# Kernel tuning notes

Measured on AMD Instinct MI355X. Metric: run time of the kernel, lower is better.

Reference implementation:

```python
import jax, jax.numpy as jnp
import numpy as np

N, E, IN, HID, H = 20000, 320000, 256, 128, 4
NEG_SLOPE = 0.2
BN_EPS = 1e-5


def _glorot(k, shape):
    lim = float(np.sqrt(6.0 / (shape[0] + shape[-1])))
    return jax.random.uniform(k, shape, jnp.float32, -lim, lim)


def setup_inputs() -> dict:
    key = jax.random.key(0)
    ks = jax.random.split(key, 16)
    x = jax.random.normal(ks[0], (N, IN), jnp.float32)
    src = jax.random.randint(ks[1], (E,), 0, N, jnp.int32)
    dst = jax.random.randint(ks[2], (E,), 0, N, jnp.int32)
    dst = jnp.where(dst == src, (dst + 1) % N, dst)  # no pre-existing self-loops
    edge_index = jnp.stack([src, dst])
    p = {}
    i = 3
    for l, fin in [(0, IN), (1, HID)]:
        p[f"Wl{l}"] = _glorot(ks[i], (fin, H * HID)); i += 1
        p[f"Wr{l}"] = _glorot(ks[i], (fin, H * HID)); i += 1
        p[f"bl{l}"] = jnp.zeros((H * HID,), jnp.float32)
        p[f"br{l}"] = jnp.zeros((H * HID,), jnp.float32)
        p[f"att{l}"] = _glorot(ks[i], (H, HID)); i += 1
        p[f"b{l}"] = jnp.zeros((HID,), jnp.float32)
        p[f"g{l}"] = jnp.ones((HID,), jnp.float32)
        p[f"be{l}"] = jnp.zeros((HID,), jnp.float32)
    p["skip_W"] = _glorot(ks[i], (IN, HID))
    p["skip_b"] = jnp.zeros((HID,), jnp.float32)
    return {"x": x, "edge_index": edge_index, **p}


def _gatv2(x, src, dst, Wl, bl, Wr, br, att, b, n):
    # PyG GATv2Conv, heads=H, concat=False (mean over heads), eval mode (no dropout)
    xl = (x @ Wl + bl).reshape(n, H, HID)   # lin_l (source)
    xr = (x @ Wr + br).reshape(n, H, HID)   # lin_r (target)
    m = xl[src] + xr[dst]                   # [Etot,H,C]
    e = jnp.einsum('ehc,hc->eh', jax.nn.leaky_relu(m, NEG_SLOPE), att)
    emax = jax.ops.segment_max(e, dst, num_segments=n)
    a = jnp.exp(e - emax[dst])
    denom = jax.ops.segment_sum(a, dst, num_segments=n)
    alpha = a / denom[dst]                  # per-target softmax over incoming edges
    out = jax.ops.segment_sum(alpha[:, :, None] * xl[src], dst, num_segments=n)
    return out.mean(axis=1) + b


def _bn(x, g, be):
    # BatchNorm1d, training-mode batch statistics (biased variance)
    mu = x.mean(0)
    var = x.var(0)
    return (x - mu) * jax.lax.rsqrt(var + BN_EPS) * g + be


def reference(x, edge_index, Wl0, Wr0, bl0, br0, att0, b0, g0, be0,
              Wl1, Wr1, bl1, br1, att1, b1, g1, be1, skip_W, skip_b):
    n = x.shape[0]
    loop = jnp.arange(n, dtype=edge_index.dtype)  # add_self_loops (GATv2 default)
    src = jnp.concatenate([edge_index[0], loop])
    dst = jnp.concatenate([edge_index[1], loop])
    h = x @ skip_W + skip_b
    out = _gatv2(x, src, dst, Wl0, bl0, Wr0, br0, att0, b0, n)
    out = _bn(jax.nn.leaky_relu(out, NEG_SLOPE), g0, be0) + h
    out = _gatv2(out, src, dst, Wl1, bl1, Wr1, br1, att1, b1, n)
    out = _bn(jax.nn.leaky_relu(out, NEG_SLOPE), g1, be1)
    return out
```

## Files before the change

kernel.cpp:

```cpp
#include <hip/hip_runtime.h>
#include <math.h>

#define NEG 0.2f
#define BN_EPS 1e-5f
#define LOG2E 1.44269504088896340736f

typedef __attribute__((ext_vector_type(8))) short  bf16x8;
typedef __attribute__((ext_vector_type(4))) float  f32x4;

__device__ inline unsigned short f2b(float f) {
    unsigned int u = __float_as_uint(f);
    unsigned int r = (u + 0x7fffu + ((u >> 16) & 1u)) >> 16;
    return (unsigned short)r;
}
__device__ inline float b2f_lo(unsigned int u) { return __uint_as_float(u << 16); }
__device__ inline float b2f_hi(unsigned int u) { return __uint_as_float(u & 0xffff0000u); }

__device__ inline unsigned int cvt_pk_bf16(float lo, float hi) {
    unsigned int r;
    asm("v_cvt_pk_bf16_f32 %0, %1, %2" : "=v"(r) : "v"(lo), "v"(hi));
    return r;
}

template<int CTRL>
__device__ inline float dpp_add(float x) {
    int y = __builtin_amdgcn_update_dpp(0, __float_as_int(x), CTRL, 0xF, 0xF, true);
    return x + __int_as_float(y);
}

__global__ void hist_kernel(const int* __restrict__ dst, int* __restrict__ counts, int E4) {
    int i = blockIdx.x * 256 + threadIdx.x;
    if (i >= E4) return;
    int4 d = ((const int4*)dst)[i];
    atomicAdd(&counts[d.x], 1);
    atomicAdd(&counts[d.y], 1);
    atomicAdd(&counts[d.z], 1);
    atomicAdd(&counts[d.w], 1);
}

__global__ void pscan_kernel(const int* __restrict__ counts, int* __restrict__ offsets,
                             int* __restrict__ btot, int n) {
    __shared__ int wsums[16];
    int tid = threadIdx.x, wid = tid >> 6, lane = tid & 63;
    int i = blockIdx.x * 1024 + tid;
    int v = (i < n) ? counts[i] + 1 : 0;
    int incl = v;
#pragma unroll
    for (int off = 1; off < 64; off <<= 1) {
        int t = __shfl_up(incl, off);
        if (lane >= off) incl += t;
    }
    if (lane == 63) wsums[wid] = incl;
    __syncthreads();
    if (tid < 16) {
        int wv = wsums[tid];
        int winc = wv;
#pragma unroll
        for (int off = 1; off < 16; off <<= 1) {
            int t = __shfl_up(winc, off);
            if (tid >= off) winc += t;
        }
        wsums[tid] = winc - wv;
        if (tid == 15) btot[blockIdx.x] = winc;
    }
    __syncthreads();
    if (i < n) offsets[i] = wsums[wid] + incl - v;
}

__global__ void addb_kernel(int* __restrict__ offsets, const int* __restrict__ btot,
                            int n, int nb) {
    __shared__ int sbase;
    if (threadIdx.x == 0) {
        int b = 0, t = 0;
        for (int j = 0; j < nb; ++j) {
            int v = btot[j];
            if (j < (int)blockIdx.x) b += v;
            t += v;
        }
        sbase = b;
        if (blockIdx.x == (unsigned)(nb - 1)) offsets[n] = t;
    }
    __syncthreads();
    int i = blockIdx.x * 1024 + threadIdx.x;
    if (i < n) offsets[i] += sbase;
}

__global__ void scatter_kernel(const int* __restrict__ src, const int* __restrict__ dst,
                               const int* __restrict__ offsets, int* __restrict__ cursor,
                               int* __restrict__ csr_src, int E, int N) {
    int i = blockIdx.x * 256 + threadIdx.x;
    if (i < E) {
        int d = dst[i];
        int pos = offsets[d] + 1 + atomicAdd(&cursor[d], 1);
        csr_src[pos] = src[i];
    } else if (i < E + N) {
        int n = i - E;
        csr_src[offsets[n]] = n;
    }
}

__device__ inline void pack_body(const float* __restrict__ W, unsigned short* __restrict__ Ap,
                                 int K, int Nsrc, int fn_off, int t) {
    int KS = K >> 5;
    int lane = t & 63;
    int frag = t >> 6;
    int ks = frag % KS;
    int nb = frag / KS;
    int fn = fn_off + nb;
    int k0 = ks * 32 + (lane >> 4) * 8;
    int col = nb * 16 + (lane & 15);
    unsigned short o[8];
#pragma unroll
    for (int j = 0; j < 8; ++j) o[j] = f2b(W[(size_t)(k0 + j) * Nsrc + col]);
    *(uint4*)&Ap[(((size_t)fn * KS + ks) * 64 + lane) * 8] = *(uint4*)o;
}

__global__ void prep_kernel(const float* __restrict__ x, unsigned short* __restrict__ xb,
                            const float* __restrict__ Wl0, const float* __restrict__ Wr0,
                            const float* __restrict__ skW, const float* __restrict__ Wl1,
                            const float* __restrict__ Wr1,
                            unsigned short* __restrict__ Ap0, unsigned short* __restrict__ Ap1,
                            const float* __restrict__ bl0, const float* __restrict__ br0,
                            const float* __restrict__ skb, const float* __restrict__ bl1,
                            const float* __restrict__ br1,
                            float* __restrict__ bias0f, float* __restrict__ bias1f, int N) {
    const int CONV = (N * 256 / 8) / 256;
    int b = blockIdx.x, tid = threadIdx.x;
    if (b < CONV) {
        int i = b * 256 + tid;
        const float4* p = (const float4*)&x[(size_t)i * 8];
        float4 a = p[0], c = p[1];
        unsigned short o[8];
        o[0] = f2b(a.x); o[1] = f2b(a.y); o[2] = f2b(a.z); o[3] = f2b(a.w);
        o[4] = f2b(c.x); o[5] = f2b(c.y); o[6] = f2b(c.z); o[7] = f2b(c.w);
        *(uint4*)&xb[(size_t)i * 8] = *(uint4*)o;
        return;
    }
    b -= CONV;
    if (b < 64)  { pack_body(Wl0, Ap0, 256, 512, 0,  b * 256 + tid); return; }
    b -= 64;
    if (b < 64)  { pack_body(Wr0, Ap0, 256, 512, 32, b * 256 + tid); return; }
    b -= 64;
    if (b < 16)  { pack_body(skW, Ap0, 256, 128, 64, b * 256 + tid); return; }
    b -= 16;
    if (b < 32)  { pack_body(Wl1, Ap1, 128, 512, 0,  b * 256 + tid); return; }
    b -= 32;
    if (b < 32)  { pack_body(Wr1, Ap1, 128, 512, 32, b * 256 + tid); return; }
    b -= 32;
    {
        int i = b * 256 + tid;
        if (i < 1152) {
            float v = (i < 512) ? bl0[i] : (i < 1024 ? br0[i - 512] : skb[i - 1024]);
            bias0f[i] = v;
        } else if (i < 1152 + 1024) {
            int j = i - 1152;
            bias1f[j] = (j < 512) ? bl1[j] : br1[j - 512];
        }
    }
}

__global__ __launch_bounds__(256) void gemm_nt(
    const unsigned short* __restrict__ Bx, const unsigned short* __restrict__ Ap,
    const float* __restrict__ bias, unsigned short* __restrict__ out,
    int Mnodes, int Ncols, int K) {
    int wid = threadIdx.x >> 6, lane = threadIdx.x & 63;
    int g = lane >> 4, c15 = lane & 15;
    int cfbase = blockIdx.y * 8 + (wid & 1) * 4;
    int ch0 = cfbase * 16;
    int nodeBase = blockIdx.x * 256 + (wid >> 1) * 128;
    const int KS = K >> 5;

    f32x4 acc[4][8];
#pragma unroll
    for (int i = 0; i < 4; ++i)
#pragma unroll
        for (int j = 0; j < 8; ++j) acc[i][j] = (f32x4){0.f, 0.f, 0.f, 0.f};

    int nd[8];
    const unsigned short* brow[8];
#pragma unroll
    for (int nf = 0; nf < 8; ++nf) {
        int n = nodeBase + nf * 16 + c15;
        nd[nf] = n;
        int nc = n < Mnodes ? n : Mnodes - 1;
        brow[nf] = Bx + (size_t)nc * K + g * 8;
    }

    for (int ks = 0; ks < KS; ++ks) {
        int koff = ks * 32;
        bf16x8 a[4];
#pragma unroll
        for (int mf = 0; mf < 4; ++mf)
            a[mf] = *(const bf16x8*)&Ap[(((size_t)(cfbase + mf) * KS + ks) * 64 + lane) * 8];
        bf16x8 b[8];
#pragma unroll
        for (int nf = 0; nf < 8; ++nf)
            b[nf] = *(const bf16x8*)(brow[nf] + koff);
#pragma unroll
        for (int nf = 0; nf < 8; ++nf)
#pragma unroll
            for (int mf = 0; mf < 4; ++mf)
                acc[mf][nf] = __builtin_amdgcn_mfma_f32_16x16x32_bf16(a[mf], b[nf], acc[mf][nf], 0, 0, 0);
    }
#pragma unroll
    for (int mf = 0; mf < 4; ++mf) {
        int ch = ch0 + mf * 16 + g * 4;
        float4 bs = *(const float4*)&bias[ch];
#pragma unroll
        for (int nf = 0; nf < 8; ++nf) {
            f32x4 v = acc[mf][nf];
            unsigned int p0 = cvt_pk_bf16(v[0] + bs.x, v[1] + bs.y);
            unsigned int p1 = cvt_pk_bf16(v[2] + bs.z, v[3] + bs.w);
            if (nd[nf] < Mnodes)
                *(uint2*)&out[(size_t)nd[nf] * Ncols + ch] = make_uint2(p0, p1);
        }
    }
}

__global__ __launch_bounds__(128) void gat_edge_kernel(
    const int* __restrict__ offsets, const int* __restrict__ csr_src,
    const unsigned short* __restrict__ base, int stride,
    const float* __restrict__ att, const float* __restrict__ bvec,
    float* __restrict__ prebn, int N) {
    int lane = threadIdx.x & 63;
    int n = blockIdx.x * 2 + (threadIdx.x >> 6);
    if (n >= N) return;
    int start = offsets[n], e1 = offsets[n + 1] - 1;
    float xrv[8], ca[8], cb[8], bv[8];
    {
        uint4 u = *(const uint4*)&base[(size_t)n * stride + 512 + lane * 8];
        xrv[0] = b2f_lo(u.x); xrv[1] = b2f_hi(u.x);
        xrv[2] = b2f_lo(u.y); xrv[3] = b2f_hi(u.y);
        xrv[4] = b2f_lo(u.z); xrv[5] = b2f_hi(u.z);
        xrv[6] = b2f_lo(u.w); xrv[7] = b2f_hi(u.w);
        const float4* q = (const float4*)&att[lane * 8];
        float4 u0 = q[0], u1 = q[1];
        const float sA = 0.6f * LOG2E, sB = 0.4f * LOG2E;
        ca[0] = u0.x * sA; ca[1] = u0.y * sA; ca[2] = u0.z * sA; ca[3] = u0.w * sA;
        ca[4] = u1.x * sA; ca[5] = u1.y * sA; ca[6] = u1.z * sA; ca[7] = u1.w * sA;
        cb[0] = u0.x * sB; cb[1] = u0.y * sB; cb[2] = u0.z * sB; cb[3] = u0.w * sB;
        cb[4] = u1.x * sB; cb[5] = u1.y * sB; cb[6] = u1.z * sB; cb[7] = u1.w * sB;
        if (lane < 16) {
            const float4* bp = (const float4*)&bvec[lane * 8];
            float4 b0 = bp[0], b1 = bp[1];
            bv[0] = b0.x; bv[1] = b0.y; bv[2] = b0.z; bv[3] = b0.w;
            bv[4] = b1.x; bv[5] = b1.y; bv[6] = b1.z; bv[7] = b1.w;
        }
    }
    float m = -INFINITY, d = 0.f;
    float acc[8] = {0, 0, 0, 0, 0, 0, 0, 0};

    const int lofs = lane * 8;
    auto LD = [&](int j) -> uint4 {
        int jj = j < e1 ? j : e1;
        int s = csr_src[jj];
        return *(const uint4*)&base[(size_t)s * stride + lofs];
    };
    auto PROC = [&](const uint4& Q) {
        float v[8];
        v[0] = b2f_lo(Q.x); v[1] = b2f_hi(Q.x);
        v[2] = b2f_lo(Q.y); v[3] = b2f_hi(Q.y);
        v[4] = b2f_lo(Q.z); v[5] = b2f_hi(Q.z);
        v[6] = b2f_lo(Q.w); v[7] = b2f_hi(Q.w);
        float p = 0.f;
#pragma unroll
        for (int j = 0; j < 8; ++j) {
            float t = v[j] + xrv[j];
            p = fmaf(ca[j], t, fmaf(cb[j], fabsf(t), p));
        }
        p = dpp_add<0xB1>(p);
        p = dpp_add<0x4E>(p);
        p = dpp_add<0x141>(p);
        p = dpp_add<0x140>(p);
        if (__any(p > m)) {
            float mn = fmaxf(m, p);
            float scale = exp2f(m - mn);
            float w = exp2f(p - mn);
            d = fmaf(d, scale, w);
#pragma unroll
            for (int j = 0; j < 8; ++j) acc[j] = fmaf(w, v[j], acc[j] * scale);
            m = mn;
        } else {
            float w = exp2f(p - m);
            d += w;
#pragma unroll
            for (int j = 0; j < 8; ++j) acc[j] = fmaf(w, v[j], acc[j]);
        }
    };

    uint4 q0 = LD(start), q1 = LD(start + 1), q2 = LD(start + 2), q3 = LD(start + 3);
    int i = start;
    for (;;) {
        PROC(q0); if (++i > e1) break; q0 = LD(i + 3);
        PROC(q1); if (++i > e1) break; q1 = LD(i + 3);
        PROC(q2); if (++i > e1) break; q2 = LD(i + 3);
        PROC(q3); if (++i > e1) break; q3 = LD(i + 3);
    }

    float inv = 1.f / d;
    float t[8];
#pragma unroll
    for (int j = 0; j < 8; ++j) {
        float u = acc[j] * inv;
        u += __shfl_xor(u, 16);
        u += __shfl_xor(u, 32);
        t[j] = u;
    }
    if (lane < 16) {
        float o[8];
#pragma unroll
        for (int j = 0; j < 8; ++j) {
            float v2 = 0.25f * t[j] + bv[j];
            o[j] = v2 > 0.f ? v2 : NEG * v2;
        }
        float* dstp = &prebn[(size_t)n * 128 + lane * 8];
        *(float4*)&dstp[0] = make_float4(o[0], o[1], o[2], o[3]);
        *(float4*)&dstp[4] = make_float4(o[4], o[5], o[6], o[7]);
    }
}

__global__ void bn_stats_kernel(const float* __restrict__ v, float* __restrict__ stats, int N) {
    int c = threadIdx.x;
    int r0 = blockIdx.x * 40;
    int r1 = r0 + 40; if (r1 > N) r1 = N;
    float s = 0.f, ss = 0.f;
    for (int r = r0; r < r1; ++r) {
        float x = v[(size_t)r * 128 + c];
        s += x; ss += x * x;
    }
    atomicAdd(&stats[c], s);
    atomicAdd(&stats[128 + c], ss);
}

__global__ void bn_apply0_kernel(const float* __restrict__ v, const float* __restrict__ stats,
                                 const float* __restrict__ g, const float* __restrict__ be,
                                 const unsigned short* __restrict__ skip16, int skipStride,
                                 unsigned short* __restrict__ out16, int N) {
    int t = blockIdx.x * 256 + threadIdx.x;
    if (t >= N * 16) return;
    int node = t >> 4, c = (t & 15) * 8;
    float invN = 1.f / (float)N;
    float4 s0 = *(const float4*)&stats[c],       s1 = *(const float4*)&stats[c + 4];
    float4 q0 = *(const float4*)&stats[128 + c], q1 = *(const float4*)&stats[128 + c + 4];
    float4 g0 = *(const float4*)&g[c],  g1 = *(const float4*)&g[c + 4];
    float4 e0 = *(const float4*)&be[c], e1 = *(const float4*)&be[c + 4];
    float mu[8]   = {s0.x, s0.y, s0.z, s0.w, s1.x, s1.y, s1.z, s1.w};
    float ssum[8] = {q0.x, q0.y, q0.z, q0.w, q1.x, q1.y, q1.z, q1.w};
    float gg[8]   = {g0.x, g0.y, g0.z, g0.w, g1.x, g1.y, g1.z, g1.w};
    float ee[8]   = {e0.x, e0.y, e0.z, e0.w, e1.x, e1.y, e1.z, e1.w};
    const float4* vp = (const float4*)&v[(size_t)node * 128 + c];
    float4 v0 = vp[0], v1 = vp[1];
    float xv[8] = {v0.x, v0.y, v0.z, v0.w, v1.x, v1.y, v1.z, v1.w};
    uint4 sk = *(const uint4*)&skip16[(size_t)node * skipStride + c];
    float skf[8] = {b2f_lo(sk.x), b2f_hi(sk.x), b2f_lo(sk.y), b2f_hi(sk.y),
                    b2f_lo(sk.z), b2f_hi(sk.z), b2f_lo(sk.w), b2f_hi(sk.w)};
    unsigned short o[8];
#pragma unroll
    for (int j = 0; j < 8; ++j) {
        float muj = mu[j] * invN;
        float var = ssum[j] * invN - muj * muj;
        float rs = rsqrtf(var + BN_EPS);
        o[j] = f2b((xv[j] - muj) * rs * gg[j] + ee[j] + skf[j]);
    }
    *(uint4*)&out16[(size_t)node * 128 + c] = *(uint4*)o;
}

__global__ void bn_apply1_kernel(const float* __restrict__ v, const float* __restrict__ stats,
                                 const float* __restrict__ g, const float* __restrict__ be,
                                 float* __restrict__ outf, int N) {
    int t = blockIdx.x * 256 + threadIdx.x;
    if (t >= N * 16) return;
    int node = t >> 4, c = (t & 15) * 8;
    float invN = 1.f / (float)N;
    const float4* vp = (const float4*)&v[(size_t)node * 128 + c];
    float4 v0 = vp[0], v1 = vp[1];
    float xv[8] = {v0.x, v0.y, v0.z, v0.w, v1.x, v1.y, v1.z, v1.w};
    float4 s0 = *(const float4*)&stats[c],       s1 = *(const float4*)&stats[c + 4];
    float4 q0 = *(const float4*)&stats[128 + c], q1 = *(const float4*)&stats[128 + c + 4];
    float4 g0 = *(const float4*)&g[c],  g1 = *(const float4*)&g[c + 4];
    float4 e0 = *(const float4*)&be[c], e1 = *(const float4*)&be[c + 4];
    float mu[8]   = {s0.x, s0.y, s0.z, s0.w, s1.x, s1.y, s1.z, s1.w};
    float ssum[8] = {q0.x, q0.y, q0.z, q0.w, q1.x, q1.y, q1.z, q1.w};
    float gg[8]   = {g0.x, g0.y, g0.z, g0.w, g1.x, g1.y, g1.z, g1.w};
    float ee[8]   = {e0.x, e0.y, e0.z, e0.w, e1.x, e1.y, e1.z, e1.w};
    float o[8];
#pragma unroll
    for (int j = 0; j < 8; ++j) {
        float muj = mu[j] * invN;
        float var = ssum[j] * invN - muj * muj;
        float rs = rsqrtf(var + BN_EPS);
        o[j] = (xv[j] - muj) * rs * gg[j] + ee[j];
    }
    float4* op = (float4*)&outf[(size_t)node * 128 + c];
    op[0] = make_float4(o[0], o[1], o[2], o[3]);
    op[1] = make_float4(o[4], o[5], o[6], o[7]);
}

extern "C" void kernel_launch(void* const* d_in, const int* in_sizes, int n_in,
                              void* d_out, int out_size, void* d_ws, size_t ws_size,
                              hipStream_t stream) {
    const float* x    = (const float*)d_in[0];
    const int*   ei   = (const int*)d_in[1];
    const float* Wl0  = (const float*)d_in[2];
    const float* Wr0  = (const float*)d_in[3];
    const float* bl0  = (const float*)d_in[4];
    const float* br0  = (const float*)d_in[5];
    const float* att0 = (const float*)d_in[6];
    const float* b0   = (const float*)d_in[7];
    const float* g0   = (const float*)d_in[8];
    const float* be0  = (const float*)d_in[9];
    const float* Wl1  = (const float*)d_in[10];
    const float* Wr1  = (const float*)d_in[11];
    const float* bl1  = (const float*)d_in[12];
    const float* br1  = (const float*)d_in[13];
    const float* att1 = (const float*)d_in[14];
    const float* b1   = (const float*)d_in[15];
    const float* g1   = (const float*)d_in[16];
    const float* be1  = (const float*)d_in[17];
    const float* skW  = (const float*)d_in[18];
    const float* skb  = (const float*)d_in[19];

    const int K0 = 256, K1 = 128;
    int N = in_sizes[0] / K0;
    int E = in_sizes[1] / 2;
    int Etot = E + N;
    int NB = (N + 1023) / 1024;

    char* ws = (char*)d_ws;
    size_t off = 0;
    auto alloc = [&](size_t bytes) { size_t r = off; off += (bytes + 255) & ~(size_t)255; return r; };
    size_t z0 = off;
    int*   counts  = (int*)(ws + alloc((size_t)N * 4));
    int*   cursor  = (int*)(ws + alloc((size_t)N * 4));
    float* stats   = (float*)(ws + alloc(512 * 4));
    size_t z1 = off;
    int*   offsets = (int*)(ws + alloc((size_t)(N + 1) * 4));
    int*   csr_src = (int*)(ws + alloc((size_t)Etot * 4));
    int*   btot    = (int*)(ws + alloc((size_t)NB * 4));
    unsigned short* xb    = (unsigned short*)(ws + alloc((size_t)N * 256 * 2));
    unsigned short* l0out = (unsigned short*)(ws + alloc((size_t)N * 128 * 2));
    float* prebn   = (float*)(ws + alloc((size_t)N * 128 * 4));
    unsigned short* fused0 = (unsigned short*)(ws + alloc((size_t)N * 1152 * 2));
    unsigned short* fused1 = fused0;
    unsigned short* Ap0 = (unsigned short*)(ws + alloc((size_t)(1152 / 16) * (K0 / 32) * 64 * 8 * 2));
    unsigned short* Ap1 = (unsigned short*)(ws + alloc((size_t)(1024 / 16) * (K1 / 32) * 64 * 8 * 2));
    float* bias0f = (float*)(ws + alloc(1152 * 4));
    float* bias1f = (float*)(ws + alloc(1024 * 4));
    float* outf = (float*)d_out;

    const int* src = ei;
    const int* dst = ei + E;

    hipMemsetAsync(ws + z0, 0, z1 - z0, stream);

    hist_kernel<<<(E / 4 + 255) / 256, 256, 0, stream>>>(dst, counts, E / 4);
    pscan_kernel<<<NB, 1024, 0, stream>>>(counts, offsets, btot, N);
    addb_kernel<<<NB, 1024, 0, stream>>>(offsets, btot, N, NB);
    scatter_kernel<<<(Etot + 255) / 256, 256, 0, stream>>>(src, dst, offsets, cursor, csr_src, E, N);

    {
        int CONV = (N * 256 / 8) / 256;
        int nblk = CONV + 64 + 64 + 16 + 32 + 32 + 9;
        prep_kernel<<<nblk, 256, 0, stream>>>(x, xb, Wl0, Wr0, skW, Wl1, Wr1, Ap0, Ap1,
                                              bl0, br0, skb, bl1, br1, bias0f, bias1f, N);
    }

    {
        dim3 g((N + 255) / 256, 1152 / 128);
        gemm_nt<<<g, 256, 0, stream>>>(xb, Ap0, bias0f, fused0, N, 1152, K0);
    }
    gat_edge_kernel<<<(N + 1) / 2, 128, 0, stream>>>(offsets, csr_src, fused0, 1152, att0, b0, prebn, N);
    bn_stats_kernel<<<(N + 39) / 40, 128, 0, stream>>>(prebn, stats, N);
    bn_apply0_kernel<<<(N * 16 + 255) / 256, 256, 0, stream>>>(
        prebn, stats, g0, be0, fused0 + 1024, 1152, l0out, N);

    {
        dim3 g((N + 255) / 256, 1024 / 128);
        gemm_nt<<<g, 256, 0, stream>>>(l0out, Ap1, bias1f, fused1, N, 1024, K1);
    }
    gat_edge_kernel<<<(N + 1) / 2, 128, 0, stream>>>(offsets, csr_src, fused1, 1024, att1, b1, prebn, N);
    bn_stats_kernel<<<(N + 39) / 40, 128, 0, stream>>>(prebn, stats + 256, N);
    bn_apply1_kernel<<<(N * 16 + 255) / 256, 256, 0, stream>>>(
        prebn, stats + 256, g1, be1, outf, N);
}
```

Baseline: 305.9 us.

## Pre-swizzle GEMM B operand into MFMA fragments, fold histogram into prep, pack edge math

The producers of the GEMM B input (prep conversion of x and the layer-0 BN apply) now write bf16 data already arranged in MFMA fragment order. This lets gemm_nt load each fragment with a single contiguous 16-byte read per lane instead of strided row reads. The edge histogram is merged into prep_kernel, removing one launch. The GAT edge inner loop is rewritten with 2-wide float vectors so the compiler can use packed FP32 instructions. The fragment layout relies on N being a multiple of 16, and the hard-coded 313 histogram blocks assume E=320000.

```diff
diff --git a/kernel.cpp b/kernel.cpp
--- a/kernel.cpp
+++ b/kernel.cpp
@@ -7,6 +7,7 @@
 
 typedef __attribute__((ext_vector_type(8))) short  bf16x8;
 typedef __attribute__((ext_vector_type(4))) float  f32x4;
+typedef __attribute__((ext_vector_type(2))) float  f32x2;
 
 __device__ inline unsigned short f2b(float f) {
     unsigned int u = __float_as_uint(f);
@@ -26,16 +27,6 @@
 __device__ inline float dpp_add(float x) {
     int y = __builtin_amdgcn_update_dpp(0, __float_as_int(x), CTRL, 0xF, 0xF, true);
     return x + __int_as_float(y);
-}
-
-__global__ void hist_kernel(const int* __restrict__ dst, int* __restrict__ counts, int E4) {
-    int i = blockIdx.x * 256 + threadIdx.x;
-    if (i >= E4) return;
-    int4 d = ((const int4*)dst)[i];
-    atomicAdd(&counts[d.x], 1);
-    atomicAdd(&counts[d.y], 1);
-    atomicAdd(&counts[d.z], 1);
-    atomicAdd(&counts[d.w], 1);
 }
 
 __global__ void pscan_kernel(const int* __restrict__ counts, int* __restrict__ offsets,
@@ -115,7 +106,8 @@
     *(uint4*)&Ap[(((size_t)fn * KS + ks) * 64 + lane) * 8] = *(uint4*)o;
 }
 
-__global__ void prep_kernel(const float* __restrict__ x, unsigned short* __restrict__ xb,
+__global__ void prep_kernel(const float* __restrict__ x, unsigned short* __restrict__ xbf,
+                            const int* __restrict__ dst, int* __restrict__ counts, int E4,
                             const float* __restrict__ Wl0, const float* __restrict__ Wr0,
                             const float* __restrict__ skW, const float* __restrict__ Wl1,
                             const float* __restrict__ Wr1,
@@ -124,19 +116,35 @@
                             const float* __restrict__ skb, const float* __restrict__ bl1,
                             const float* __restrict__ br1,
                             float* __restrict__ bias0f, float* __restrict__ bias1f, int N) {
-    const int CONV = (N * 256 / 8) / 256;
+    const int CONV = (N / 16) * 8 / 4;
     int b = blockIdx.x, tid = threadIdx.x;
+    int wid = tid >> 6, lane = tid & 63;
     if (b < CONV) {
-        int i = b * 256 + tid;
-        const float4* p = (const float4*)&x[(size_t)i * 8];
+        int wt = b * 4 + wid;
+        int ntile = wt >> 3, ks = wt & 7;
+        int r = ntile * 16 + (lane & 15);
+        int k = ks * 32 + (lane >> 4) * 8;
+        const float4* p = (const float4*)&x[(size_t)r * 256 + k];
         float4 a = p[0], c = p[1];
         unsigned short o[8];
         o[0] = f2b(a.x); o[1] = f2b(a.y); o[2] = f2b(a.z); o[3] = f2b(a.w);
         o[4] = f2b(c.x); o[5] = f2b(c.y); o[6] = f2b(c.z); o[7] = f2b(c.w);
-        *(uint4*)&xb[(size_t)i * 8] = *(uint4*)o;
+        *(uint4*)&xbf[(((size_t)ntile * 8 + ks) * 64 + lane) * 8] = *(uint4*)o;
         return;
     }
     b -= CONV;
+    if (b < 313) {
+        int i = b * 256 + tid;
+        if (i < E4) {
+            int4 d = ((const int4*)dst)[i];
+            atomicAdd(&counts[d.x], 1);
+            atomicAdd(&counts[d.y], 1);
+            atomicAdd(&counts[d.z], 1);
+            atomicAdd(&counts[d.w], 1);
+        }
+        return;
+    }
+    b -= 313;
     if (b < 64)  { pack_body(Wl0, Ap0, 256, 512, 0,  b * 256 + tid); return; }
     b -= 64;
     if (b < 64)  { pack_body(Wr0, Ap0, 256, 512, 32, b * 256 + tid); return; }
@@ -160,7 +168,7 @@
 }
 
 __global__ __launch_bounds__(256) void gemm_nt(
-    const unsigned short* __restrict__ Bx, const unsigned short* __restrict__ Ap,
+    const unsigned short* __restrict__ Bf, const unsigned short* __restrict__ Ap,
     const float* __restrict__ bias, unsigned short* __restrict__ out,
     int Mnodes, int Ncols, int K) {
     int wid = threadIdx.x >> 6, lane = threadIdx.x & 63;
@@ -169,6 +177,7 @@
     int ch0 = cfbase * 16;
     int nodeBase = blockIdx.x * 256 + (wid >> 1) * 128;
     const int KS = K >> 5;
+    const int lastNT = (Mnodes - 1) >> 4;
 
     f32x4 acc[4][8];
 #pragma unroll
@@ -176,18 +185,15 @@
 #pragma unroll
         for (int j = 0; j < 8; ++j) acc[i][j] = (f32x4){0.f, 0.f, 0.f, 0.f};
 
-    int nd[8];
-    const unsigned short* brow[8];
+    int nt[8], nd[8];
 #pragma unroll
     for (int nf = 0; nf < 8; ++nf) {
-        int n = nodeBase + nf * 16 + c15;
-        nd[nf] = n;
-        int nc = n < Mnodes ? n : Mnodes - 1;
-        brow[nf] = Bx + (size_t)nc * K + g * 8;
+        int t = (nodeBase >> 4) + nf;
+        nt[nf] = t < lastNT ? t : lastNT;
+        nd[nf] = nodeBase + nf * 16 + c15;
     }
 
     for (int ks = 0; ks < KS; ++ks) {
-        int koff = ks * 32;
         bf16x8 a[4];
 #pragma unroll
         for (int mf = 0; mf < 4; ++mf)
@@ -195,7 +201,7 @@
         bf16x8 b[8];
 #pragma unroll
         for (int nf = 0; nf < 8; ++nf)
-            b[nf] = *(const bf16x8*)(brow[nf] + koff);
+            b[nf] = *(const bf16x8*)&Bf[(((size_t)nt[nf] * KS + ks) * 64 + lane) * 8];
 #pragma unroll
         for (int nf = 0; nf < 8; ++nf)
 #pragma unroll
@@ -226,20 +232,21 @@
     int n = blockIdx.x * 2 + (threadIdx.x >> 6);
     if (n >= N) return;
     int start = offsets[n], e1 = offsets[n + 1] - 1;
-    float xrv[8], ca[8], cb[8], bv[8];
+    f32x2 xr2[4], ca2[4], cb2[4];
+    float bv[8];
     {
         uint4 u = *(const uint4*)&base[(size_t)n * stride + 512 + lane * 8];
-        xrv[0] = b2f_lo(u.x); xrv[1] = b2f_hi(u.x);
-        xrv[2] = b2f_lo(u.y); xrv[3] = b2f_hi(u.y);
-        xrv[4] = b2f_lo(u.z); xrv[5] = b2f_hi(u.z);
-        xrv[6] = b2f_lo(u.w); xrv[7] = b2f_hi(u.w);
+        xr2[0] = (f32x2){b2f_lo(u.x), b2f_hi(u.x)};
+        xr2[1] = (f32x2){b2f_lo(u.y), b2f_hi(u.y)};
+        xr2[2] = (f32x2){b2f_lo(u.z), b2f_hi(u.z)};
+        xr2[3] = (f32x2){b2f_lo(u.w), b2f_hi(u.w)};
         const float4* q = (const float4*)&att[lane * 8];
         float4 u0 = q[0], u1 = q[1];
         const float sA = 0.6f * LOG2E, sB = 0.4f * LOG2E;
-        ca[0] = u0.x * sA; ca[1] = u0.y * sA; ca[2] = u0.z * sA; ca[3] = u0.w * sA;
-        ca[4] = u1.x * sA; ca[5] = u1.y * sA; ca[6] = u1.z * sA; ca[7] = u1.w * sA;
-        cb[0] = u0.x * sB; cb[1] = u0.y * sB; cb[2] = u0.z * sB; cb[3] = u0.w * sB;
-        cb[4] = u1.x * sB; cb[5] = u1.y * sB; cb[6] = u1.z * sB; cb[7] = u1.w * sB;
+        ca2[0] = (f32x2){u0.x * sA, u0.y * sA}; ca2[1] = (f32x2){u0.z * sA, u0.w * sA};
+        ca2[2] = (f32x2){u1.x * sA, u1.y * sA}; ca2[3] = (f32x2){u1.z * sA, u1.w * sA};
+        cb2[0] = (f32x2){u0.x * sB, u0.y * sB}; cb2[1] = (f32x2){u0.z * sB, u0.w * sB};
+        cb2[2] = (f32x2){u1.x * sB, u1.y * sB}; cb2[3] = (f32x2){u1.z * sB, u1.w * sB};
         if (lane < 16) {
             const float4* bp = (const float4*)&bvec[lane * 8];
             float4 b0 = bp[0], b1 = bp[1];
@@ -248,7 +255,9 @@
         }
     }
     float m = -INFINITY, d = 0.f;
-    float acc[8] = {0, 0, 0, 0, 0, 0, 0, 0};
+    f32x2 acc2[4];
+#pragma unroll
+    for (int j = 0; j < 4; ++j) acc2[j] = (f32x2){0.f, 0.f};
 
     const int lofs = lane * 8;
     auto LD = [&](int j) -> uint4 {
@@ -257,34 +266,39 @@
         return *(const uint4*)&base[(size_t)s * stride + lofs];
     };
     auto PROC = [&](const uint4& Q) {
-        float v[8];
-        v[0] = b2f_lo(Q.x); v[1] = b2f_hi(Q.x);
-        v[2] = b2f_lo(Q.y); v[3] = b2f_hi(Q.y);
-        v[4] = b2f_lo(Q.z); v[5] = b2f_hi(Q.z);
-        v[6] = b2f_lo(Q.w); v[7] = b2f_hi(Q.w);
-        float p = 0.f;
-#pragma unroll
-        for (int j = 0; j < 8; ++j) {
-            float t = v[j] + xrv[j];
-            p = fmaf(ca[j], t, fmaf(cb[j], fabsf(t), p));
-        }
+        f32x2 v0 = (f32x2){b2f_lo(Q.x), b2f_hi(Q.x)};
+        f32x2 v1 = (f32x2){b2f_lo(Q.y), b2f_hi(Q.y)};
+        f32x2 v2 = (f32x2){b2f_lo(Q.z), b2f_hi(Q.z)};
+        f32x2 v3 = (f32x2){b2f_lo(Q.w), b2f_hi(Q.w)};
+        f32x2 t0 = v0 + xr2[0], t1 = v1 + xr2[1], t2 = v2 + xr2[2], t3 = v3 + xr2[3];
+        f32x2 ps = ca2[0] * t0 + cb2[0] * __builtin_elementwise_abs(t0);
+        ps += ca2[1] * t1 + cb2[1] * __builtin_elementwise_abs(t1);
+        ps += ca2[2] * t2 + cb2[2] * __builtin_elementwise_abs(t2);
+        ps += ca2[3] * t3 + cb2[3] * __builtin_elementwise_abs(t3);
+        float p = ps.x + ps.y;
         p = dpp_add<0xB1>(p);
         p = dpp_add<0x4E>(p);
         p = dpp_add<0x141>(p);
         p = dpp_add<0x140>(p);
         if (__any(p > m)) {
             float mn = fmaxf(m, p);
-            float scale = exp2f(m - mn);
+            float sc = exp2f(m - mn);
             float w = exp2f(p - mn);
-            d = fmaf(d, scale, w);
-#pragma unroll
-            for (int j = 0; j < 8; ++j) acc[j] = fmaf(w, v[j], acc[j] * scale);
+            d = fmaf(d, sc, w);
+            f32x2 w2 = (f32x2){w, w}, sc2 = (f32x2){sc, sc};
+            acc2[0] = w2 * v0 + acc2[0] * sc2;
+            acc2[1] = w2 * v1 + acc2[1] * sc2;
+            acc2[2] = w2 * v2 + acc2[2] * sc2;
+            acc2[3] = w2 * v3 + acc2[3] * sc2;
             m = mn;
         } else {
             float w = exp2f(p - m);
             d += w;
-#pragma unroll
-            for (int j = 0; j < 8; ++j) acc[j] = fmaf(w, v[j], acc[j]);
+            f32x2 w2 = (f32x2){w, w};
+            acc2[0] += w2 * v0;
+            acc2[1] += w2 * v1;
+            acc2[2] += w2 * v2;
+            acc2[3] += w2 * v3;
         }
     };
 
@@ -298,13 +312,15 @@
     }
 
     float inv = 1.f / d;
+    f32x2 inv2 = (f32x2){inv, inv};
     float t[8];
 #pragma unroll
-    for (int j = 0; j < 8; ++j) {
-        float u = acc[j] * inv;
-        u += __shfl_xor(u, 16);
-        u += __shfl_xor(u, 32);
-        t[j] = u;
+    for (int jp = 0; jp < 4; ++jp) {
+        f32x2 u2 = acc2[jp] * inv2;
+        float ua = u2.x, ub = u2.y;
+        ua += __shfl_xor(ua, 16); ua += __shfl_xor(ua, 32);
+        ub += __shfl_xor(ub, 16); ub += __shfl_xor(ub, 32);
+        t[jp * 2] = ua; t[jp * 2 + 1] = ub;
     }
     if (lane < 16) {
         float o[8];
@@ -332,13 +348,16 @@
     atomicAdd(&stats[128 + c], ss);
 }
 
-__global__ void bn_apply0_kernel(const float* __restrict__ v, const float* __restrict__ stats,
-                                 const float* __restrict__ g, const float* __restrict__ be,
-                                 const unsigned short* __restrict__ skip16, int skipStride,
-                                 unsigned short* __restrict__ out16, int N) {
-    int t = blockIdx.x * 256 + threadIdx.x;
-    if (t >= N * 16) return;
-    int node = t >> 4, c = (t & 15) * 8;
+__global__ void bn_apply_frag_kernel(const float* __restrict__ v, const float* __restrict__ stats,
+                                     const float* __restrict__ g, const float* __restrict__ be,
+                                     const unsigned short* __restrict__ skip16, int skipStride,
+                                     unsigned short* __restrict__ outf, int N) {
+    int wid = threadIdx.x >> 6, lane = threadIdx.x & 63;
+    int wt = blockIdx.x * 4 + wid;
+    int ntile = wt >> 2, ks = wt & 3;
+    int r = ntile * 16 + (lane & 15);
+    if (r >= N) return;
+    int c = ks * 32 + (lane >> 4) * 8;
     float invN = 1.f / (float)N;
     float4 s0 = *(const float4*)&stats[c],       s1 = *(const float4*)&stats[c + 4];
     float4 q0 = *(const float4*)&stats[128 + c], q1 = *(const float4*)&stats[128 + c + 4];
@@ -348,10 +367,10 @@
     float ssum[8] = {q0.x, q0.y, q0.z, q0.w, q1.x, q1.y, q1.z, q1.w};
     float gg[8]   = {g0.x, g0.y, g0.z, g0.w, g1.x, g1.y, g1.z, g1.w};
     float ee[8]   = {e0.x, e0.y, e0.z, e0.w, e1.x, e1.y, e1.z, e1.w};
-    const float4* vp = (const float4*)&v[(size_t)node * 128 + c];
+    const float4* vp = (const float4*)&v[(size_t)r * 128 + c];
     float4 v0 = vp[0], v1 = vp[1];
     float xv[8] = {v0.x, v0.y, v0.z, v0.w, v1.x, v1.y, v1.z, v1.w};
-    uint4 sk = *(const uint4*)&skip16[(size_t)node * skipStride + c];
+    uint4 sk = *(const uint4*)&skip16[(size_t)r * skipStride + c];
     float skf[8] = {b2f_lo(sk.x), b2f_hi(sk.x), b2f_lo(sk.y), b2f_hi(sk.y),
                     b2f_lo(sk.z), b2f_hi(sk.z), b2f_lo(sk.w), b2f_hi(sk.w)};
     unsigned short o[8];
@@ -362,7 +381,7 @@
         float rs = rsqrtf(var + BN_EPS);
         o[j] = f2b((xv[j] - muj) * rs * gg[j] + ee[j] + skf[j]);
     }
-    *(uint4*)&out16[(size_t)node * 128 + c] = *(uint4*)o;
+    *(uint4*)&outf[(((size_t)ntile * 4 + ks) * 64 + lane) * 8] = *(uint4*)o;
 }
 
 __global__ void bn_apply1_kernel(const float* __restrict__ v, const float* __restrict__ stats,
@@ -437,8 +456,8 @@
     int*   offsets = (int*)(ws + alloc((size_t)(N + 1) * 4));
     int*   csr_src = (int*)(ws + alloc((size_t)Etot * 4));
     int*   btot    = (int*)(ws + alloc((size_t)NB * 4));
-    unsigned short* xb    = (unsigned short*)(ws + alloc((size_t)N * 256 * 2));
-    unsigned short* l0out = (unsigned short*)(ws + alloc((size_t)N * 128 * 2));
+    unsigned short* xbf   = (unsigned short*)(ws + alloc((size_t)N * 256 * 2));
+    unsigned short* l0f   = (unsigned short*)(ws + alloc((size_t)N * 128 * 2));
     float* prebn   = (float*)(ws + alloc((size_t)N * 128 * 4));
     unsigned short* fused0 = (unsigned short*)(ws + alloc((size_t)N * 1152 * 2));
     unsigned short* fused1 = fused0;
@@ -453,30 +472,29 @@
 
     hipMemsetAsync(ws + z0, 0, z1 - z0, stream);
 
-    hist_kernel<<<(E / 4 + 255) / 256, 256, 0, stream>>>(dst, counts, E / 4);
+    {
+        int CONV = (N / 16) * 8 / 4;
+        int nblk = CONV + 313 + 64 + 64 + 16 + 32 + 32 + 9;
+        prep_kernel<<<nblk, 256, 0, stream>>>(x, xbf, dst, counts, E / 4,
+                                              Wl0, Wr0, skW, Wl1, Wr1, Ap0, Ap1,
+                                              bl0, br0, skb, bl1, br1, bias0f, bias1f, N);
+    }
     pscan_kernel<<<NB, 1024, 0, stream>>>(counts, offsets, btot, N);
     addb_kernel<<<NB, 1024, 0, stream>>>(offsets, btot, N, NB);
     scatter_kernel<<<(Etot + 255) / 256, 256, 0, stream>>>(src, dst, offsets, cursor, csr_src, E, N);
 
     {
-        int CONV = (N * 256 / 8) / 256;
-        int nblk = CONV + 64 + 64 + 16 + 32 + 32 + 9;
-        prep_kernel<<<nblk, 256, 0, stream>>>(x, xb, Wl0, Wr0, skW, Wl1, Wr1, Ap0, Ap1,
-                                              bl0, br0, skb, bl1, br1, bias0f, bias1f, N);
-    }
-
-    {
         dim3 g((N + 255) / 256, 1152 / 128);
-        gemm_nt<<<g, 256, 0, stream>>>(xb, Ap0, bias0f, fused0, N, 1152, K0);
+        gemm_nt<<<g, 256, 0, stream>>>(xbf, Ap0, bias0f, fused0, N, 1152, K0);
     }
     gat_edge_kernel<<<(N + 1) / 2, 128, 0, stream>>>(offsets, csr_src, fused0, 1152, att0, b0, prebn, N);
     bn_stats_kernel<<<(N + 39) / 40, 128, 0, stream>>>(prebn, stats, N);
-    bn_apply0_kernel<<<(N * 16 + 255) / 256, 256, 0, stream>>>(
-        prebn, stats, g0, be0, fused0 + 1024, 1152, l0out, N);
+    bn_apply_frag_kernel<<<(N / 16), 256, 0, stream>>>(
+        prebn, stats, g0, be0, fused0 + 1024, 1152, l0f, N);
 
     {
         dim3 g((N + 255) / 256, 1024 / 128);
-        gemm_nt<<<g, 256, 0, stream>>>(l0out, Ap1, bias1f, fused1, N, 1024, K1);
+        gemm_nt<<<g, 256, 0, stream>>>(l0f, Ap1, bias1f, fused1, N, 1024, K1);
     }
     gat_edge_kernel<<<(N + 1) / 2, 128, 0, stream>>>(offsets, csr_src, fused1, 1024, att1, b1, prebn, N);
     bn_stats_kernel<<<(N + 39) / 40, 128, 0, stream>>>(prebn, stats + 256, N);
```

Measured after the change: 299.2 us. 2.2% less time.
